# Performance work log

Hardware: AMD Instinct MI355X
Metric: run time of the kernel (lower is better)

## Reference

```python
import jax, jax.numpy as jnp
import numpy as np

N = 8192
D_IN, D_H, D_OUT = 512, 256, 128
BETA = 0.8
EPS = 1e-08


def _xavier(key, fan_in, fan_out):
    limit = float(np.sqrt(6.0 / (fan_in + fan_out)))
    return jax.random.uniform(key, (fan_in, fan_out), jnp.float32, -limit, limit)


def setup_inputs() -> dict:
    key = jax.random.key(0)
    kA, kS, kx, kw1, kw2 = jax.random.split(key, 5)
    A = jax.random.uniform(kA, (N, N), jnp.float32)
    S = jax.random.uniform(kS, (N, N), jnp.float32)
    x = jax.random.normal(kx, (N, D_IN), jnp.float32)
    W1 = _xavier(kw1, D_IN, D_H)
    b1 = jnp.zeros((D_H,), jnp.float32)
    W2 = _xavier(kw2, D_H, D_OUT)
    b2 = jnp.zeros((D_OUT,), jnp.float32)
    return {"A": A, "S": S, "x": x, "W1": W1, "b1": b1, "W2": W2, "b2": b2}


def _normalize_adj(adj):
    # adj + eps * I  (add only on the diagonal; no dense eye materialized)
    idx = jnp.arange(adj.shape[0])
    adj = adj.at[idx, idx].add(EPS)
    d = adj.sum(axis=1)                       # [N]
    d_inv_sqrt = d ** -0.5
    d_inv_sqrt = jnp.where(jnp.isinf(d_inv_sqrt), 0.0, d_inv_sqrt)
    # D^{-1/2} A D^{-1/2} as broadcast row/col scaling (same math as diag matmuls)
    return d_inv_sqrt[:, None] * adj * d_inv_sqrt[None, :]


def reference(A, S, x, W1, b1, W2, b2):
    A_tilde = A + BETA * S                    # [N, N]
    A_norm = _normalize_adj(A_tilde)          # [N, N]
    # GCN layer 1: relu(A_norm @ (x @ W1) + b1)   (dropout is identity at eval)
    h = jax.nn.relu(A_norm @ (x @ W1) + b1)   # [N, D_H]
    # GCN layer 2 (output layer, no activation)
    out = A_norm @ (h @ W2) + b2              # [N, D_OUT]
    return out
```

## Files before the change

kernel.cpp:

```cpp
#include <hip/hip_runtime.h>

#define EPS 1e-8f
#define BETA 0.8f

typedef __attribute__((ext_vector_type(8))) short bf16x8;
typedef __attribute__((ext_vector_type(4))) float f32x4;
typedef __attribute__((ext_vector_type(4))) float float4v;
typedef __attribute__((ext_vector_type(4))) unsigned short ushort4v;

__device__ __forceinline__ unsigned short f2b(float f) {
  unsigned int u = __builtin_bit_cast(unsigned int, f);
  u += 0x7fffu + ((u >> 16) & 1u);
  return (unsigned short)(u >> 16);
}

__global__ __launch_bounds__(256) void k_degree_convert(
    const float* __restrict__ A, const float* __restrict__ S,
    unsigned short* __restrict__ At, float* __restrict__ dis) {
  const int row = blockIdx.x;
  const int tid = threadIdx.x;
  const size_t base = (size_t)row * 8192;
  float4v a[8], s[8];
#pragma unroll
  for (int i = 0; i < 8; ++i) {
    const int c = i * 1024 + tid * 4;
    a[i] = __builtin_nontemporal_load(
        reinterpret_cast<const float4v*>(A + base + c));
    s[i] = __builtin_nontemporal_load(
        reinterpret_cast<const float4v*>(S + base + c));
  }
  float sum = 0.f;
#pragma unroll
  for (int i = 0; i < 8; ++i) {
    const int c = i * 1024 + tid * 4;
    float v0 = a[i].x + BETA * s[i].x;
    float v1 = a[i].y + BETA * s[i].y;
    float v2 = a[i].z + BETA * s[i].z;
    float v3 = a[i].w + BETA * s[i].w;
    sum += (v0 + v1) + (v2 + v3);
    ushort4v o = {f2b(v0), f2b(v1), f2b(v2), f2b(v3)};
    *reinterpret_cast<ushort4v*>(At + base + c) = o;
  }
#pragma unroll
  for (int off = 32; off > 0; off >>= 1) sum += __shfl_xor(sum, off, 64);
  __shared__ float wsum[4];
  if ((tid & 63) == 0) wsum[tid >> 6] = sum;
  __syncthreads();
  if (tid == 0) {
    float d = ((wsum[0] + wsum[1]) + (wsum[2] + wsum[3])) + EPS;
    dis[row] = (d > 0.f) ? 1.0f / sqrtf(d) : 0.f;
  }
}

__global__ __launch_bounds__(256) void k_conv_bf16(
    const float* __restrict__ in, unsigned short* __restrict__ out, int n4) {
  int idx = blockIdx.x * 256 + threadIdx.x;
  if (idx >= n4) return;
  float4v v = reinterpret_cast<const float4v*>(in)[idx];
  ushort4v o = {f2b(v.x), f2b(v.y), f2b(v.z), f2b(v.w)};
  reinterpret_cast<ushort4v*>(out)[idx] = o;
}

__global__ __launch_bounds__(256) void k_convT(
    const float* __restrict__ W, unsigned short* __restrict__ WT, int R, int C) {
  int idx = blockIdx.x * 256 + threadIdx.x;
  if (idx >= R * C) return;
  int r = idx / C, c = idx - r * C;
  WT[c * R + r] = f2b(W[idx]);
}

template <int BM, int BN, int EPI>
__global__ __launch_bounds__(256) void k_gemm_bt(
    const unsigned short* __restrict__ Ag, const unsigned short* __restrict__ BTg,
    int M, int N, int Kstride, int Kchunk,
    const float* __restrict__ dis, const float* __restrict__ bias,
    float* __restrict__ outf, unsigned short* __restrict__ outb) {
  constexpr int WM = BM / 2, WN = BN / 2;
  constexpr int MF = WM / 16, NF = WN / 16;
  constexpr int NLOADS = BM / 32 + BN / 32;
  __shared__ unsigned short Als[2][BM][64];
  __shared__ unsigned short Bls[2][BN][64];
  const int tid = threadIdx.x;
  const int lane = tid & 63;
  const int wm = (tid >> 6) >> 1, wn = (tid >> 6) & 1;
  const int brow = blockIdx.x * BM, bcol = blockIdx.y * BN;
  const int ar = tid >> 3;
  const int ac = (tid & 7) * 8;
  const int l15 = lane & 15, lk = (lane >> 4) * 8;

  f32x4 acc[MF][NF];
#pragma unroll
  for (int i = 0; i < MF; ++i)
#pragma unroll
    for (int j = 0; j < NF; ++j) acc[i][j] = (f32x4){0.f, 0.f, 0.f, 0.f};

  auto stage = [&](int buf, int k0) {
#pragma unroll
    for (int i = 0; i < BM / 32; ++i) {
      const unsigned short* g =
          Ag + (size_t)(brow + i * 32 + ar) * Kstride + k0 + ac;
      __builtin_amdgcn_global_load_lds(
          (const __attribute__((address_space(1))) void*)g,
          (__attribute__((address_space(3))) void*)&Als[buf][i * 32 + ar][ac],
          16, 0, 0);
    }
#pragma unroll
    for (int i = 0; i < BN / 32; ++i) {
      const unsigned short* g =
          BTg + (size_t)(bcol + i * 32 + ar) * Kstride + k0 + ac;
      __builtin_amdgcn_global_load_lds(
          (const __attribute__((address_space(1))) void*)g,
          (__attribute__((address_space(3))) void*)&Bls[buf][i * 32 + ar][ac],
          16, 0, 0);
    }
  };

  const int nsteps = Kchunk / 64;
  stage(0, 0);
  for (int t = 0; t < nsteps; ++t) {
    const int cur = t & 1;
    if (t + 1 < nsteps) {
      stage(cur ^ 1, (t + 1) * 64);
      asm volatile("s_waitcnt vmcnt(%0)" ::"n"(NLOADS));
    } else {
      asm volatile("s_waitcnt vmcnt(0)");
    }
    __builtin_amdgcn_s_barrier();
    asm volatile("" ::: "memory");
#pragma unroll
    for (int kk = 0; kk < 2; ++kk) {
      bf16x8 afr[MF], bfr[NF];
#pragma unroll
      for (int mi = 0; mi < MF; ++mi)
        afr[mi] = *reinterpret_cast<const bf16x8*>(
            &Als[cur][wm * WM + mi * 16 + l15][kk * 32 + lk]);
#pragma unroll
      for (int ni = 0; ni < NF; ++ni)
        bfr[ni] = *reinterpret_cast<const bf16x8*>(
            &Bls[cur][wn * WN + ni * 16 + l15][kk * 32 + lk]);
#pragma unroll
      for (int mi = 0; mi < MF; ++mi)
#pragma unroll
        for (int ni = 0; ni < NF; ++ni)
          acc[mi][ni] = __builtin_amdgcn_mfma_f32_16x16x32_bf16(
              afr[mi], bfr[ni], acc[mi][ni], 0, 0, 0);
    }
    asm volatile("" ::: "memory");
    __builtin_amdgcn_s_barrier();
  }

  const int crow0 = brow + wm * WM, ccol0 = bcol + wn * WN;
#pragma unroll
  for (int mi = 0; mi < MF; ++mi) {
    const int row0 = crow0 + mi * 16 + (lane >> 4) * 4;
    const float d0 = dis[row0], d1 = dis[row0 + 1], d2 = dis[row0 + 2],
                d3 = dis[row0 + 3];
#pragma unroll
    for (int ni = 0; ni < NF; ++ni) {
      const int col = ccol0 + ni * 16 + l15;
      f32x4 a = acc[mi][ni];
      if constexpr (EPI == 0) {
        ushort4v o = {f2b(d0 * a.x), f2b(d1 * a.y), f2b(d2 * a.z),
                      f2b(d3 * a.w)};
        *reinterpret_cast<ushort4v*>(outb + (size_t)col * M + row0) = o;
      } else if constexpr (EPI == 1) {
        const float bb = bias[col];
        float v0 = d0 * a.x + bb; v0 = v0 > 0.f ? v0 : 0.f;
        float v1 = d1 * a.y + bb; v1 = v1 > 0.f ? v1 : 0.f;
        float v2 = d2 * a.z + bb; v2 = v2 > 0.f ? v2 : 0.f;
        float v3 = d3 * a.w + bb; v3 = v3 > 0.f ? v3 : 0.f;
        outb[(size_t)(row0 + 0) * N + col] = f2b(v0);
        outb[(size_t)(row0 + 1) * N + col] = f2b(v1);
        outb[(size_t)(row0 + 2) * N + col] = f2b(v2);
        outb[(size_t)(row0 + 3) * N + col] = f2b(v3);
      } else {
        const float bb = bias[col];
        outf[(size_t)(row0 + 0) * N + col] = d0 * a.x + bb;
        outf[(size_t)(row0 + 1) * N + col] = d1 * a.y + bb;
        outf[(size_t)(row0 + 2) * N + col] = d2 * a.z + bb;
        outf[(size_t)(row0 + 3) * N + col] = d3 * a.w + bb;
      }
    }
  }
}

__global__ __launch_bounds__(512, 4) void k_gemm_big(
    const unsigned short* __restrict__ Ag,
    const unsigned short* __restrict__ BTg,
    int M, int N, int Kstride, int Kchunk,
    float* __restrict__ P) {
  constexpr int BM = 256, BN = 64;
  constexpr int MF = 4, NF = 2;
  constexpr int NLOADS = 5;
  __shared__ unsigned short Als[2][BM][64];
  __shared__ unsigned short Bls[2][BN][64];
  const int tid = threadIdx.x;
  const int lane = tid & 63;
  const int wid = tid >> 6;
  const int wm = wid >> 1, wn = wid & 1;
  const int brow = blockIdx.x * BM, bcol = blockIdx.y * BN;
  const int kbase = blockIdx.z * Kchunk;
  const int ar = tid >> 3;
  const int ac = (tid & 7) * 8;
  const int l15 = lane & 15, lk = (lane >> 4) * 8;

  f32x4 acc[MF][NF];
#pragma unroll
  for (int i = 0; i < MF; ++i)
#pragma unroll
    for (int j = 0; j < NF; ++j) acc[i][j] = (f32x4){0.f, 0.f, 0.f, 0.f};

  auto stage = [&](int buf, int k0) {
#pragma unroll
    for (int i = 0; i < 4; ++i) {
      const unsigned short* g =
          Ag + (size_t)(brow + i * 64 + ar) * Kstride + k0 + ac;
      __builtin_amdgcn_global_load_lds(
          (const __attribute__((address_space(1))) void*)g,
          (__attribute__((address_space(3))) void*)&Als[buf][i * 64 + ar][ac],
          16, 0, 0);
    }
    {
      const unsigned short* g = BTg + (size_t)(bcol + ar) * Kstride + k0 + ac;
      __builtin_amdgcn_global_load_lds(
          (const __attribute__((address_space(1))) void*)g,
          (__attribute__((address_space(3))) void*)&Bls[buf][ar][ac], 16, 0, 0);
    }
  };

  const int nsteps = Kchunk / 64;
  stage(0, kbase);
  for (int t = 0; t < nsteps; ++t) {
    const int cur = t & 1;
    if (t + 1 < nsteps) {
      stage(cur ^ 1, kbase + (t + 1) * 64);
      asm volatile("s_waitcnt vmcnt(%0)" ::"n"(NLOADS));
    } else {
      asm volatile("s_waitcnt vmcnt(0)");
    }
    __builtin_amdgcn_s_barrier();
    asm volatile("" ::: "memory");
#pragma unroll
    for (int kk = 0; kk < 2; ++kk) {
      bf16x8 afr[MF], bfr[NF];
#pragma unroll
      for (int mi = 0; mi < MF; ++mi)
        afr[mi] = *reinterpret_cast<const bf16x8*>(
            &Als[cur][wm * 64 + mi * 16 + l15][kk * 32 + lk]);
#pragma unroll
      for (int ni = 0; ni < NF; ++ni)
        bfr[ni] = *reinterpret_cast<const bf16x8*>(
            &Bls[cur][wn * 32 + ni * 16 + l15][kk * 32 + lk]);
#pragma unroll
      for (int mi = 0; mi < MF; ++mi)
#pragma unroll
        for (int ni = 0; ni < NF; ++ni)
          acc[mi][ni] = __builtin_amdgcn_mfma_f32_16x16x32_bf16(
              afr[mi], bfr[ni], acc[mi][ni], 0, 0, 0);
    }
    asm volatile("" ::: "memory");
    __builtin_amdgcn_s_barrier();
  }

  float* Pz = P + (size_t)blockIdx.z * M * N;
  const int crow0 = brow + wm * 64, ccol0 = bcol + wn * 32;
#pragma unroll
  for (int mi = 0; mi < MF; ++mi) {
    const int row0 = crow0 + mi * 16 + (lane >> 4) * 4;
#pragma unroll
    for (int ni = 0; ni < NF; ++ni) {
      const int col = ccol0 + ni * 16 + l15;
      f32x4 a = acc[mi][ni];
      Pz[(size_t)(row0 + 0) * N + col] = a.x;
      Pz[(size_t)(row0 + 1) * N + col] = a.y;
      Pz[(size_t)(row0 + 2) * N + col] = a.z;
      Pz[(size_t)(row0 + 3) * N + col] = a.w;
    }
  }
}

template <int MODE, int NS>
__global__ __launch_bounds__(256) void k_reduceN(
    const float* __restrict__ P, int M, int N,
    const float* __restrict__ dis, const float* __restrict__ bias,
    unsigned short* __restrict__ outb, float* __restrict__ outf) {
  const int idx = blockIdx.x * 256 + threadIdx.x;
  const int row = idx / (N / 4);
  const int c0 = (idx - row * (N / 4)) * 4;
  const size_t off = (size_t)row * N + c0;
  const size_t ps = (size_t)M * N;
  float r0 = 0.f, r1 = 0.f, r2 = 0.f, r3 = 0.f;
#pragma unroll
  for (int z = 0; z < NS; ++z) {
    float4v v = *reinterpret_cast<const float4v*>(P + z * ps + off);
    r0 += v.x; r1 += v.y; r2 += v.z; r3 += v.w;
  }
  const float d = dis[row];
  float4v bb = *reinterpret_cast<const float4v*>(bias + c0);
  r0 = d * r0 + bb.x; r1 = d * r1 + bb.y;
  r2 = d * r2 + bb.z; r3 = d * r3 + bb.w;
  if constexpr (MODE == 0) {
    r0 = r0 > 0.f ? r0 : 0.f;
    r1 = r1 > 0.f ? r1 : 0.f;
    r2 = r2 > 0.f ? r2 : 0.f;
    r3 = r3 > 0.f ? r3 : 0.f;
    ushort4v o = {f2b(r0), f2b(r1), f2b(r2), f2b(r3)};
    *reinterpret_cast<ushort4v*>(outb + off) = o;
  } else {
    float4v o = {r0, r1, r2, r3};
    *reinterpret_cast<float4v*>(outf + off) = o;
  }
}

extern "C" void kernel_launch(void* const* d_in, const int* in_sizes, int n_in,
                              void* d_out, int out_size, void* d_ws,
                              size_t ws_size, hipStream_t stream) {
  const float* A  = (const float*)d_in[0];
  const float* S  = (const float*)d_in[1];
  const float* x  = (const float*)d_in[2];
  const float* W1 = (const float*)d_in[3];
  const float* b1 = (const float*)d_in[4];
  const float* W2 = (const float*)d_in[5];
  const float* b2 = (const float*)d_in[6];
  float* out = (float*)d_out;

  char* ws = (char*)d_ws;
  dim3 blk(256);

  const size_t O_At = 0, O_xb = 134217728, O_M1T = 142606336,
               O_P = 146800640, O_W1T = 180355072, O_W2T = 180617216,
               O_dis = 180682752, NEED = 180715520;

  if (ws_size >= NEED) {
    unsigned short* At  = (unsigned short*)(ws + O_At);
    unsigned short* xb  = (unsigned short*)(ws + O_xb);
    unsigned short* M1T = (unsigned short*)(ws + O_M1T);
    float*          P   = (float*)(ws + O_P);
    unsigned short* hb  = (unsigned short*)(ws + O_M1T);
    unsigned short* M2T = (unsigned short*)(ws + O_xb);
    unsigned short* W1T = (unsigned short*)(ws + O_W1T);
    unsigned short* W2T = (unsigned short*)(ws + O_W2T);
    float*          dis = (float*)(ws + O_dis);

    k_degree_convert<<<8192, blk, 0, stream>>>(A, S, At, dis);
    k_conv_bf16<<<4096, blk, 0, stream>>>(x, xb, 4194304 / 4);
    k_convT<<<512, blk, 0, stream>>>(W1, W1T, 512, 256);
    k_convT<<<128, blk, 0, stream>>>(W2, W2T, 256, 128);
    k_gemm_bt<128, 64, 0><<<dim3(64, 4), blk, 0, stream>>>(
        xb, W1T, 8192, 256, 512, 512, dis, nullptr, nullptr, M1T);
    k_gemm_big<<<dim3(32, 4, 4), dim3(512), 0, stream>>>(
        At, M1T, 8192, 256, 8192, 2048, P);
    k_reduceN<0, 4><<<2048, blk, 0, stream>>>(P, 8192, 256, dis, b1, hb,
                                              nullptr);
    k_gemm_bt<64, 64, 0><<<dim3(128, 2), blk, 0, stream>>>(
        hb, W2T, 8192, 128, 256, 256, dis, nullptr, nullptr, M2T);
    k_gemm_big<<<dim3(32, 2, 8), dim3(512), 0, stream>>>(
        At, M2T, 8192, 128, 8192, 1024, P);
    k_reduceN<1, 8><<<1024, blk, 0, stream>>>(P, 8192, 128, dis, b2, nullptr,
                                              out);
  } else {
    unsigned short* At  = (unsigned short*)(ws);
    unsigned short* xb  = (unsigned short*)(ws + 134217728);
    unsigned short* M1T = (unsigned short*)(ws + 142606336);
    unsigned short* hb  = (unsigned short*)(ws + 146800640);
    unsigned short* M2T = (unsigned short*)(ws + 150994944);
    unsigned short* W1T = (unsigned short*)(ws + 153092096);
    unsigned short* W2T = (unsigned short*)(ws + 153354240);
    float* dis          = (float*)(ws + 153419776);

    k_degree_convert<<<8192, blk, 0, stream>>>(A, S, At, dis);
    k_conv_bf16<<<4096, blk, 0, stream>>>(x, xb, 4194304 / 4);
    k_convT<<<512, blk, 0, stream>>>(W1, W1T, 512, 256);
    k_convT<<<128, blk, 0, stream>>>(W2, W2T, 256, 128);
    k_gemm_bt<128, 64, 0><<<dim3(64, 4), blk, 0, stream>>>(
        xb, W1T, 8192, 256, 512, 512, dis, nullptr, nullptr, M1T);
    k_gemm_bt<128, 64, 1><<<dim3(64, 4), blk, 0, stream>>>(
        At, M1T, 8192, 256, 8192, 8192, dis, b1, nullptr, hb);
    k_gemm_bt<64, 64, 0><<<dim3(128, 2), blk, 0, stream>>>(
        hb, W2T, 8192, 128, 256, 256, dis, nullptr, nullptr, M2T);
    k_gemm_bt<64, 64, 2><<<dim3(128, 2), blk, 0, stream>>>(
        At, M2T, 8192, 128, 8192, 8192, dis, b2, out, nullptr);
  }
}
```

Before: 233.4 us.

## Cover full N width per block in split-K adjacency GEMMs with XCD swizzle

Result: no change. 236.9 us (+1.5%).

```diff
diff --git a/kernel.cpp b/kernel.cpp
--- a/kernel.cpp
+++ b/kernel.cpp
@@ -184,35 +184,42 @@
   }
 }
 
-__global__ __launch_bounds__(512, 4) void k_gemm_big(
+template <int BM, int BN, int WGM, int WGN>
+__global__ __launch_bounds__(512, 2) void k_gemm_split(
     const unsigned short* __restrict__ Ag,
     const unsigned short* __restrict__ BTg,
-    int M, int N, int Kstride, int Kchunk,
+    int M, int N, int Kstride, int Kchunk, int gx,
     float* __restrict__ P) {
-  constexpr int BM = 256, BN = 64;
-  constexpr int MF = 4, NF = 2;
-  constexpr int NLOADS = 5;
+  constexpr int NLOADS = BM / 64 + BN / 64;
   __shared__ unsigned short Als[2][BM][64];
   __shared__ unsigned short Bls[2][BN][64];
+
+  const int nblk = gridDim.x;
+  const int flat = blockIdx.x;
+  const int cpx = nblk >> 3;
+  const int swz = (flat & 7) * cpx + (flat >> 3);
+  const int bx = swz % gx;
+  const int bz = swz / gx;
+
   const int tid = threadIdx.x;
   const int lane = tid & 63;
   const int wid = tid >> 6;
-  const int wm = wid >> 1, wn = wid & 1;
-  const int brow = blockIdx.x * BM, bcol = blockIdx.y * BN;
-  const int kbase = blockIdx.z * Kchunk;
+  const int wm = wid / WGN, wn = wid % WGN;
+  const int brow = bx * BM;
+  const int kbase = bz * Kchunk;
   const int ar = tid >> 3;
   const int ac = (tid & 7) * 8;
   const int l15 = lane & 15, lk = (lane >> 4) * 8;
 
-  f32x4 acc[MF][NF];
-#pragma unroll
-  for (int i = 0; i < MF; ++i)
-#pragma unroll
-    for (int j = 0; j < NF; ++j) acc[i][j] = (f32x4){0.f, 0.f, 0.f, 0.f};
+  f32x4 acc[4][4];
+#pragma unroll
+  for (int i = 0; i < 4; ++i)
+#pragma unroll
+    for (int j = 0; j < 4; ++j) acc[i][j] = (f32x4){0.f, 0.f, 0.f, 0.f};
 
   auto stage = [&](int buf, int k0) {
 #pragma unroll
-    for (int i = 0; i < 4; ++i) {
+    for (int i = 0; i < BM / 64; ++i) {
       const unsigned short* g =
           Ag + (size_t)(brow + i * 64 + ar) * Kstride + k0 + ac;
       __builtin_amdgcn_global_load_lds(
@@ -220,11 +227,13 @@
           (__attribute__((address_space(3))) void*)&Als[buf][i * 64 + ar][ac],
           16, 0, 0);
     }
-    {
-      const unsigned short* g = BTg + (size_t)(bcol + ar) * Kstride + k0 + ac;
+#pragma unroll
+    for (int i = 0; i < BN / 64; ++i) {
+      const unsigned short* g = BTg + (size_t)(i * 64 + ar) * Kstride + k0 + ac;
       __builtin_amdgcn_global_load_lds(
           (const __attribute__((address_space(1))) void*)g,
-          (__attribute__((address_space(3))) void*)&Bls[buf][ar][ac], 16, 0, 0);
+          (__attribute__((address_space(3))) void*)&Bls[buf][i * 64 + ar][ac],
+          16, 0, 0);
     }
   };
 
@@ -242,19 +251,19 @@
     asm volatile("" ::: "memory");
 #pragma unroll
     for (int kk = 0; kk < 2; ++kk) {
-      bf16x8 afr[MF], bfr[NF];
-#pragma unroll
-      for (int mi = 0; mi < MF; ++mi)
+      bf16x8 afr[4], bfr[4];
+#pragma unroll
+      for (int mi = 0; mi < 4; ++mi)
         afr[mi] = *reinterpret_cast<const bf16x8*>(
             &Als[cur][wm * 64 + mi * 16 + l15][kk * 32 + lk]);
 #pragma unroll
-      for (int ni = 0; ni < NF; ++ni)
+      for (int ni = 0; ni < 4; ++ni)
         bfr[ni] = *reinterpret_cast<const bf16x8*>(
-            &Bls[cur][wn * 32 + ni * 16 + l15][kk * 32 + lk]);
-#pragma unroll
-      for (int mi = 0; mi < MF; ++mi)
-#pragma unroll
-        for (int ni = 0; ni < NF; ++ni)
+            &Bls[cur][wn * 64 + ni * 16 + l15][kk * 32 + lk]);
+#pragma unroll
+      for (int mi = 0; mi < 4; ++mi)
+#pragma unroll
+        for (int ni = 0; ni < 4; ++ni)
           acc[mi][ni] = __builtin_amdgcn_mfma_f32_16x16x32_bf16(
               afr[mi], bfr[ni], acc[mi][ni], 0, 0, 0);
     }
@@ -262,13 +271,13 @@
     __builtin_amdgcn_s_barrier();
   }
 
-  float* Pz = P + (size_t)blockIdx.z * M * N;
-  const int crow0 = brow + wm * 64, ccol0 = bcol + wn * 32;
-#pragma unroll
-  for (int mi = 0; mi < MF; ++mi) {
+  float* Pz = P + (size_t)bz * M * N;
+  const int crow0 = brow + wm * 64, ccol0 = wn * 64;
+#pragma unroll
+  for (int mi = 0; mi < 4; ++mi) {
     const int row0 = crow0 + mi * 16 + (lane >> 4) * 4;
 #pragma unroll
-    for (int ni = 0; ni < NF; ++ni) {
+    for (int ni = 0; ni < 4; ++ni) {
       const int col = ccol0 + ni * 16 + l15;
       f32x4 a = acc[mi][ni];
       Pz[(size_t)(row0 + 0) * N + col] = a.x;
@@ -348,14 +357,14 @@
     k_convT<<<128, blk, 0, stream>>>(W2, W2T, 256, 128);
     k_gemm_bt<128, 64, 0><<<dim3(64, 4), blk, 0, stream>>>(
         xb, W1T, 8192, 256, 512, 512, dis, nullptr, nullptr, M1T);
-    k_gemm_big<<<dim3(32, 4, 4), dim3(512), 0, stream>>>(
-        At, M1T, 8192, 256, 8192, 2048, P);
+    k_gemm_split<128, 256, 2, 4><<<dim3(256), dim3(512), 0, stream>>>(
+        At, M1T, 8192, 256, 8192, 2048, 64, P);
     k_reduceN<0, 4><<<2048, blk, 0, stream>>>(P, 8192, 256, dis, b1, hb,
                                               nullptr);
     k_gemm_bt<64, 64, 0><<<dim3(128, 2), blk, 0, stream>>>(
         hb, W2T, 8192, 128, 256, 256, dis, nullptr, nullptr, M2T);
-    k_gemm_big<<<dim3(32, 2, 8), dim3(512), 0, stream>>>(
-        At, M2T, 8192, 128, 8192, 1024, P);
+    k_gemm_split<256, 128, 4, 2><<<dim3(256), dim3(512), 0, stream>>>(
+        At, M2T, 8192, 128, 8192, 1024, 32, P);
     k_reduceN<1, 8><<<1024, blk, 0, stream>>>(P, 8192, 128, dis, b2, nullptr,
                                               out);
   } else {
```
